# Kernel tuning notes

Measured on AMD Instinct MI355X. Metric: run time of the kernel, lower is better.

## Reference

```python
import jax, jax.numpy as jnp
import numpy as np

B, N, K = 4, 8192, 16
C_IN, C1, C2, C3 = 256, 128, 128, 64
WN = 8  # weight-net hidden channels

def _leaky(x):
    return jnp.where(x >= 0, x, 0.1 * x)

def _gather(x, idx):
    # x: [B, C, N], idx: [B, N, K] -> [B, C, N, K]
    return jax.vmap(lambda xb, ib: xb[:, ib])(x, idx)

def _point_conv(xyz, feat, knn, w_wn, b_wn, w_lin, b_lin):
    # xyz [B,3,N], feat [B,C,N] -> [B,out,N]
    f = jnp.concatenate([xyz, feat], axis=1)              # [B, C+3, N]
    fg = _gather(f, knn)                                  # [B, C+3, N, K]
    pos = _gather(xyz, knn) - xyz[:, :, :, None]          # [B, 3, N, K] relative coords
    w = _leaky(jnp.einsum('mc,bcnk->bmnk', w_wn, pos) + b_wn[None, :, None, None])  # [B,WN,N,K]
    agg = jnp.einsum('bcnk,bmnk->bncm', fg, w)            # [B, N, C+3, WN]
    agg = agg.reshape(agg.shape[0], agg.shape[1], -1)     # [B, N, (C+3)*WN]
    out = _leaky(jnp.einsum('bnf,of->bno', agg, w_lin) + b_lin)
    return out.transpose(0, 2, 1)                         # [B, out, N]

def _conv1x1(x, w, b):
    return jnp.einsum('oc,bcn->bon', w, x) + b[None, :, None]

def setup_inputs():
    key = jax.random.key(0)
    ks = jax.random.split(key, 16)
    def wn(k, shape, fan_in):
        return jax.random.normal(k, shape, jnp.float32) / np.sqrt(fan_in).astype(np.float32)
    return {
        'xyz': jax.random.normal(ks[0], (B, 3, N), jnp.float32),
        'feat': jax.random.normal(ks[1], (B, C_IN, N), jnp.float32),
        'knn_indices': jax.random.randint(ks[2], (B, N, K), 0, N, dtype=jnp.int32),
        'w_wn1': wn(ks[3], (WN, 3), 3), 'b_wn1': jnp.zeros((WN,), jnp.float32),
        'w_lin1': wn(ks[4], (C1, WN * (C_IN + 3)), WN * (C_IN + 3)), 'b_lin1': jnp.zeros((C1,), jnp.float32),
        'w_wn2': wn(ks[5], (WN, 3), 3), 'b_wn2': jnp.zeros((WN,), jnp.float32),
        'w_lin2': wn(ks[6], (C2, WN * (C1 + 3)), WN * (C1 + 3)), 'b_lin2': jnp.zeros((C2,), jnp.float32),
        'w_mlp1': wn(ks[7], (C2, C2), C2), 'b_mlp1': jnp.zeros((C2,), jnp.float32),
        'w_mlp2': wn(ks[8], (C3, C2), C2), 'b_mlp2': jnp.zeros((C3,), jnp.float32),
        'w_last': wn(ks[9], (3, C3), C3), 'b_last': jnp.zeros((3,), jnp.float32),
    }

def reference(xyz, feat, knn_indices, w_wn1, b_wn1, w_lin1, b_lin1,
              w_wn2, b_wn2, w_lin2, b_lin2, w_mlp1, b_mlp1,
              w_mlp2, b_mlp2, w_last, b_last):
    f = _point_conv(xyz, feat, knn_indices, w_wn1, b_wn1, w_lin1, b_lin1)
    f = _point_conv(xyz, f, knn_indices, w_wn2, b_wn2, w_lin2, b_lin2)
    f = _leaky(_conv1x1(f, w_mlp1, b_mlp1))
    f = _leaky(_conv1x1(f, w_mlp2, b_mlp2))   # flow_feat [B, 64, N]
    flow = _conv1x1(f, w_last, b_last)        # [B, 3, N]
    return (f, flow)
```

## Files before the change

### kernel.cpp

```cpp
#include <hip/hip_runtime.h>

#define NPTS 8192
#define PTS 32768

typedef unsigned short u16;
typedef __attribute__((ext_vector_type(8))) short bf16x8;
typedef __attribute__((ext_vector_type(4))) float f32x4;

__device__ __forceinline__ float lrelu(float x){ return x >= 0.f ? x : 0.1f*x; }
__device__ __forceinline__ unsigned f2bf(float x){
  unsigned u = __float_as_uint(x);
  return ((u + 0x7FFFu + ((u>>16)&1u)) >> 16);
}
__device__ __forceinline__ float bf2f(u16 h){ return __uint_as_float(((unsigned)h)<<16); }

__global__ __launch_bounds__(256) void xyz_fill_kernel(
    const float* __restrict__ xyz, u16* __restrict__ fT1, u16* __restrict__ fT2){
  long g = (long)blockIdx.x*256 + threadIdx.x;
  int b = (int)(g >> 13), n = (int)(g & 8191);
  unsigned v[3];
  #pragma unroll
  for (int j = 0; j < 3; ++j) v[j] = f2bf(xyz[((long)b*3 + j)*NPTS + n]);
  fT1[g*264 + 0] = (u16)v[0]; fT1[g*264 + 1] = (u16)v[1]; fT1[g*264 + 2] = (u16)v[2];
  #pragma unroll
  for (int j = 259; j < 264; ++j) fT1[g*264 + j] = 0;
  uint4 u;
  u.x = v[0] | (v[1] << 16);
  u.y = v[2];
  u.z = 0; u.w = 0;
  *(uint4*)(fT2 + g*136 + 128) = u;
}

__global__ __launch_bounds__(256) void transpose_feat_kernel(
    const float* __restrict__ feat, u16* __restrict__ fT1){
  __shared__ float tile[64][65];
  int bx = blockIdx.x, by = blockIdx.y, bz = blockIdx.z;
  int t = threadIdx.x;
  int x = t & 63, y4 = t >> 6;
  const float* src = feat + ((long)bz*256 + by*64)*NPTS + (long)bx*64;
  #pragma unroll
  for (int i = 0; i < 16; ++i){
    int c = y4 + i*4;
    tile[c][x] = src[(long)c*NPTS + x];
  }
  __syncthreads();
  u16* dst = fT1 + ((long)bz*NPTS + (long)bx*64)*264 + 3 + by*64;
  #pragma unroll
  for (int i = 0; i < 16; ++i){
    int p = y4 + i*4;
    dst[(long)p*264 + x] = (u16)f2bf(tile[x][p]);
  }
}

__global__ void prep_bt_kernel(const float* __restrict__ W, u16* __restrict__ Bt,
                               int KP, int KREAL){
  int o = blockIdx.y;
  int k = blockIdx.x*256 + threadIdx.x;
  if (k < KP)
    Bt[(long)o*KP + k] = (k < KREAL) ? (u16)f2bf(W[(long)o*KREAL + k]) : (u16)0;
}

__global__ void prep_bt2_kernel(const float* __restrict__ W, u16* __restrict__ Bt){
  int o = blockIdx.y;
  int k = blockIdx.x*256 + threadIdx.x;
  if (k >= 1088) return;
  int c = k >> 3, m = k & 7;
  u16 v = 0;
  if (c < 128)      v = (u16)f2bf(W[(long)o*1048 + (c+3)*8 + m]);
  else if (c < 131) v = (u16)f2bf(W[(long)o*1048 + (c-128)*8 + m]);
  Bt[(long)o*1088 + k] = v;
}

template<int S>
__global__ __launch_bounds__(256, 2) void fused_pc_kernel(
    const u16* __restrict__ fT, const float* __restrict__ xyz,
    const int* __restrict__ knn, const float* __restrict__ w_wn,
    const float* __restrict__ b_wn, const u16* __restrict__ Bt,
    const float* __restrict__ bias, u16* __restrict__ outp, int out_stride){
  constexpr int K   = S*8;
  constexpr int NCH = S/8;
  __shared__ __align__(16) u16   As[64][72];
  __shared__ __align__(16) u16   Bs[128][72];
  __shared__ __align__(16) float fst[64*140];
  __shared__ __align__(16) u16   wk2[64][16][8];

  int t = threadIdx.x;
  int cpx = (int)(gridDim.x >> 3);
  int swz = (blockIdx.x & 7)*cpx + (blockIdx.x >> 3);
  int m0 = swz*64;
  int b = m0 >> 13;
  long bbase = (long)b << 13;
  int n0 = m0 & 8191;

  int w = t >> 6, l = t & 63;
  int ln = l & 15, lh = l >> 4;
  int o0 = w*32;

  int p = l, kb = w;
  int4 iv = *(const int4*)(knn + ((long)(bbase + n0 + p))*16 + kb*4);
  int idxs[4] = {iv.x, iv.y, iv.z, iv.w};

  {
    float cx = xyz[((long)b*3+0)*NPTS + n0 + p];
    float cy = xyz[((long)b*3+1)*NPTS + n0 + p];
    float cz = xyz[((long)b*3+2)*NPTS + n0 + p];
    float wm[8][3], bm[8];
    #pragma unroll
    for (int m = 0; m < 8; ++m){
      wm[m][0] = w_wn[m*3+0]; wm[m][1] = w_wn[m*3+1]; wm[m][2] = w_wn[m*3+2];
      bm[m] = b_wn[m];
    }
    #pragma unroll
    for (int j = 0; j < 4; ++j){
      int k = kb*4 + j;
      int idx = idxs[j];
      float px = xyz[((long)b*3+0)*NPTS + idx] - cx;
      float py = xyz[((long)b*3+1)*NPTS + idx] - cy;
      float pz = xyz[((long)b*3+2)*NPTS + idx] - cz;
      unsigned wv[8];
      #pragma unroll
      for (int m = 0; m < 8; ++m){
        float v = wm[m][0]*px + wm[m][1]*py + wm[m][2]*pz + bm[m];
        wv[m] = f2bf(lrelu(v));
      }
      uint4 u;
      u.x = wv[0] | (wv[1] << 16);
      u.y = wv[2] | (wv[3] << 16);
      u.z = wv[4] | (wv[5] << 16);
      u.w = wv[6] | (wv[7] << 16);
      *(uint4*)&wk2[p][(k + p) & 15][0] = u;
    }
  }

  uint4 ga[4];
  #pragma unroll
  for (int j = 0; j < 4; ++j)
    ga[j] = *(const uint4*)(fT + (bbase + idxs[j])*(long)S + 0*8);

  int pA = w*16 + (l >> 2), cp = l & 3;

  f32x4 acc[4][2];
  #pragma unroll
  for (int i = 0; i < 4; ++i)
    #pragma unroll
    for (int j = 0; j < 2; ++j) acc[i][j] = (f32x4){0.f,0.f,0.f,0.f};

  for (int ch = 0; ch < NCH; ++ch){
    #pragma unroll
    for (int j = 0; j < 4; ++j){
      int k = kb*4 + j;
      uint4 v = ga[j];
      f32x4 lo, hi;
      lo[0] = bf2f((u16)(v.x & 0xffff)); lo[1] = bf2f((u16)(v.x >> 16));
      lo[2] = bf2f((u16)(v.y & 0xffff)); lo[3] = bf2f((u16)(v.y >> 16));
      hi[0] = bf2f((u16)(v.z & 0xffff)); hi[1] = bf2f((u16)(v.z >> 16));
      hi[2] = bf2f((u16)(v.w & 0xffff)); hi[3] = bf2f((u16)(v.w >> 16));
      *(f32x4*)&fst[p*140 + k*8 + 0] = lo;
      *(f32x4*)&fst[p*140 + k*8 + 4] = hi;
    }
    #pragma unroll
    for (int j = 0; j < 4; ++j){
      int idx2 = j*256 + t;
      int o = idx2 >> 3, seg = (idx2 & 7)*8;
      *(uint4*)&Bs[o][seg] = *(const uint4*)(Bt + (long)o*K + ch*64 + seg);
    }
    __syncthreads();

    if (ch + 1 < NCH){
      #pragma unroll
      for (int j = 0; j < 4; ++j)
        ga[j] = *(const uint4*)(fT + (bbase + idxs[j])*(long)S + (ch+1)*8);
    }

    {
      float a0[8], a1[8];
      #pragma unroll
      for (int m = 0; m < 8; ++m){ a0[m] = 0.f; a1[m] = 0.f; }
      #pragma unroll
      for (int k = 0; k < 16; ++k){
        bf16x8 wv = *(const bf16x8*)&wk2[pA][(k + pA) & 15][0];
        const float* fr = &fst[pA*140 + k*8 + cp*2];
        float f0 = fr[0], f1 = fr[1];
        #pragma unroll
        for (int m = 0; m < 8; ++m){
          float wf = bf2f((u16)wv[m]);
          a0[m] += f0*wf;
          a1[m] += f1*wf;
        }
      }
      uint4 u0, u1;
      u0.x = f2bf(a0[0]) | (f2bf(a0[1]) << 16);
      u0.y = f2bf(a0[2]) | (f2bf(a0[3]) << 16);
      u0.z = f2bf(a0[4]) | (f2bf(a0[5]) << 16);
      u0.w = f2bf(a0[6]) | (f2bf(a0[7]) << 16);
      u1.x = f2bf(a1[0]) | (f2bf(a1[1]) << 16);
      u1.y = f2bf(a1[2]) | (f2bf(a1[3]) << 16);
      u1.z = f2bf(a1[4]) | (f2bf(a1[5]) << 16);
      u1.w = f2bf(a1[6]) | (f2bf(a1[7]) << 16);
      *(uint4*)&As[pA][cp*16 + 0] = u0;
      *(uint4*)&As[pA][cp*16 + 8] = u1;
    }
    __syncthreads();

    #pragma unroll
    for (int kk = 0; kk < 2; ++kk){
      int koff = kk*32 + lh*8;
      bf16x8 af[4], bfr[2];
      #pragma unroll
      for (int fm = 0; fm < 4; ++fm)
        af[fm] = *(const bf16x8*)&As[fm*16 + ln][koff];
      #pragma unroll
      for (int fn = 0; fn < 2; ++fn)
        bfr[fn] = *(const bf16x8*)&Bs[o0 + fn*16 + ln][koff];
      #pragma unroll
      for (int fm = 0; fm < 4; ++fm)
        #pragma unroll
        for (int fn = 0; fn < 2; ++fn)
          acc[fm][fn] = __builtin_amdgcn_mfma_f32_16x16x32_bf16(af[fm], bfr[fn], acc[fm][fn], 0, 0, 0);
    }
    __syncthreads();
  }

  u16* Cs = (u16*)fst;
  float bia[2] = { bias[o0 + ln], bias[o0 + 16 + ln] };
  #pragma unroll
  for (int fm = 0; fm < 4; ++fm)
    #pragma unroll
    for (int fn = 0; fn < 2; ++fn)
      #pragma unroll
      for (int r = 0; r < 4; ++r){
        int row = fm*16 + lh*4 + r;
        int col = o0 + fn*16 + ln;
        Cs[row*128 + col] = (u16)f2bf(lrelu(acc[fm][fn][r] + bia[fn]));
      }
  __syncthreads();
  int r2 = t >> 2, s2 = t & 3;
  u16* dst = outp + (long)(m0 + r2)*out_stride + s2*32;
  #pragma unroll
  for (int q = 0; q < 4; ++q)
    *(uint4*)(dst + q*8) = *(uint4*)&Cs[r2*128 + s2*32 + q*8];
}

template<int BN, int OUTMODE>
__global__ __launch_bounds__(256) void mfma_lin_kernel(
    const u16* __restrict__ A, const u16* __restrict__ Bt,
    const float* __restrict__ bias, void* __restrict__ outp,
    int K, long chunk_base, int out_stride){
  __shared__ __align__(16) u16 As[64][72];
  __shared__ __align__(16) u16 Bs[BN][72];
  constexpr int FM = (BN == 128) ? 4 : 2;
  int t = threadIdx.x;
  int w = t >> 6, l = t & 63;
  int ln = l & 15, lh = l >> 4;
  int m0 = blockIdx.x * 64;
  int MOFF = (BN == 128) ? 0 : (w >> 1)*32;
  int o0   = (BN == 128) ? w*32 : (w & 1)*32;
  int srow = t >> 3;
  int scol = (t & 7) * 8;

  f32x4 acc[FM][2];
  #pragma unroll
  for (int i = 0; i < FM; ++i)
    #pragma unroll
    for (int j = 0; j < 2; ++j) acc[i][j] = (f32x4){0.f,0.f,0.f,0.f};

  int nkc = K >> 6;
  for (int kc = 0; kc < nkc; ++kc){
    uint4 a0 = *(const uint4*)(A + (long)(m0 + srow)*K      + kc*64 + scol);
    uint4 a1 = *(const uint4*)(A + (long)(m0 + srow + 32)*K + kc*64 + scol);
    uint4 bv[BN/32];
    #pragma unroll
    for (int r = 0; r < BN/32; ++r)
      bv[r] = *(const uint4*)(Bt + (long)(srow + r*32)*K + kc*64 + scol);
    __syncthreads();
    *(uint4*)&As[srow][scol]      = a0;
    *(uint4*)&As[srow + 32][scol] = a1;
    #pragma unroll
    for (int r = 0; r < BN/32; ++r)
      *(uint4*)&Bs[srow + r*32][scol] = bv[r];
    __syncthreads();
    #pragma unroll
    for (int kk = 0; kk < 2; ++kk){
      int koff = kk*32 + lh*8;
      bf16x8 af[FM], bfr[2];
      #pragma unroll
      for (int fm = 0; fm < FM; ++fm)
        af[fm] = *(const bf16x8*)&As[MOFF + fm*16 + ln][koff];
      #pragma unroll
      for (int fn = 0; fn < 2; ++fn)
        bfr[fn] = *(const bf16x8*)&Bs[o0 + fn*16 + ln][koff];
      #pragma unroll
      for (int fm = 0; fm < FM; ++fm)
        #pragma unroll
        for (int fn = 0; fn < 2; ++fn)
          acc[fm][fn] = __builtin_amdgcn_mfma_f32_16x16x32_bf16(af[fm], bfr[fn], acc[fm][fn], 0, 0, 0);
    }
    __syncthreads();
  }

  if (OUTMODE == 0){
    __shared__ u16 Cs[64*128];
    float bia[2];
    #pragma unroll
    for (int fn = 0; fn < 2; ++fn) bia[fn] = bias[o0 + fn*16 + ln];
    __syncthreads();
    #pragma unroll
    for (int fm = 0; fm < FM; ++fm)
      #pragma unroll
      for (int fn = 0; fn < 2; ++fn)
        #pragma unroll
        for (int r = 0; r < 4; ++r){
          int row = MOFF + fm*16 + lh*4 + r;
          int col = o0 + fn*16 + ln;
          Cs[row*128 + col] = (u16)f2bf(lrelu(acc[fm][fn][r] + bia[fn]));
        }
    __syncthreads();
    int r2 = t >> 2, s2 = t & 3;
    u16* dst = (u16*)outp + (chunk_base + m0 + r2)*(long)out_stride + s2*32;
    #pragma unroll
    for (int q = 0; q < 4; ++q)
      *(uint4*)(dst + q*8) = *(uint4*)&Cs[r2*128 + s2*32 + q*8];
  } else {
    float* outf = (float*)outp;
    #pragma unroll
    for (int fm = 0; fm < FM; ++fm)
      #pragma unroll
      for (int fn = 0; fn < 2; ++fn){
        long gp = chunk_base + m0 + MOFF + fm*16 + lh*4;
        int bb = (int)(gp >> 13), nn = (int)(gp & 8191);
        int col = o0 + fn*16 + ln;
        float bia = bias[col];
        float4 v;
        v.x = lrelu(acc[fm][fn][0] + bia);
        v.y = lrelu(acc[fm][fn][1] + bia);
        v.z = lrelu(acc[fm][fn][2] + bia);
        v.w = lrelu(acc[fm][fn][3] + bia);
        *(float4*)(outf + ((long)(bb*64 + col) << 13) + nn) = v;
      }
  }
}

__global__ __launch_bounds__(256) void flow_kernel(
    const float* __restrict__ f, const float* __restrict__ W,
    const float* __restrict__ bias, float* __restrict__ flow){
  long g = (long)blockIdx.x*256 + threadIdx.x;
  int b = (int)(g >> 13), n = (int)(g & 8191);
  float a0 = bias[0], a1 = bias[1], a2 = bias[2];
  const float* fb = f + (long)b*64*NPTS + n;
  #pragma unroll
  for (int c = 0; c < 64; ++c){
    float v = fb[(long)c*NPTS];
    a0 += v * W[c];
    a1 += v * W[64 + c];
    a2 += v * W[128 + c];
  }
  flow[((long)b*3 + 0)*NPTS + n] = a0;
  flow[((long)b*3 + 1)*NPTS + n] = a1;
  flow[((long)b*3 + 2)*NPTS + n] = a2;
}

extern "C" void kernel_launch(void* const* d_in, const int* in_sizes, int n_in,
                              void* d_out, int out_size, void* d_ws, size_t ws_size,
                              hipStream_t stream){
  const float* xyz    = (const float*)d_in[0];
  const float* feat   = (const float*)d_in[1];
  const int*   knn    = (const int*)  d_in[2];
  const float* w_wn1  = (const float*)d_in[3];
  const float* b_wn1  = (const float*)d_in[4];
  const float* w_lin1 = (const float*)d_in[5];
  const float* b_lin1 = (const float*)d_in[6];
  const float* w_wn2  = (const float*)d_in[7];
  const float* b_wn2  = (const float*)d_in[8];
  const float* w_lin2 = (const float*)d_in[9];
  const float* b_lin2 = (const float*)d_in[10];
  const float* w_mlp1 = (const float*)d_in[11];
  const float* b_mlp1 = (const float*)d_in[12];
  const float* w_mlp2 = (const float*)d_in[13];
  const float* b_mlp2 = (const float*)d_in[14];
  const float* w_last = (const float*)d_in[15];
  const float* b_last = (const float*)d_in[16];
  float* out = (float*)d_out;

  char* p = (char*)d_ws;
  auto carve = [&](size_t bytes)->char*{
    char* r = p; p += (bytes + 255) & ~(size_t)255; return r;
  };
  u16* fT1   = (u16*)carve((size_t)PTS*264*2);
  u16* fT2   = (u16*)carve((size_t)PTS*136*2);
  u16* Bt1   = (u16*)carve((size_t)128*2112*2);
  u16* Bt2   = (u16*)carve((size_t)128*1088*2);
  u16* Bm1   = (u16*)carve((size_t)128*128*2);
  u16* Bm2   = (u16*)carve((size_t)64*128*2);
  u16* feat2 = (u16*)carve((size_t)PTS*128*2);
  u16* h1    = (u16*)carve((size_t)PTS*128*2);

  xyz_fill_kernel<<<PTS/256, 256, 0, stream>>>(xyz, fT1, fT2);
  transpose_feat_kernel<<<dim3(128,4,4), 256, 0, stream>>>(feat, fT1);
  prep_bt_kernel<<<dim3(9,128), 256, 0, stream>>>(w_lin1, Bt1, 2112, 2072);
  prep_bt2_kernel<<<dim3(5,128), 256, 0, stream>>>(w_lin2, Bt2);
  prep_bt_kernel<<<dim3(1,128), 256, 0, stream>>>(w_mlp1, Bm1, 128, 128);
  prep_bt_kernel<<<dim3(1,64),  256, 0, stream>>>(w_mlp2, Bm2, 128, 128);

  fused_pc_kernel<264><<<PTS/64, 256, 0, stream>>>(fT1, xyz, knn, w_wn1, b_wn1, Bt1, b_lin1, fT2, 136);
  fused_pc_kernel<136><<<PTS/64, 256, 0, stream>>>(fT2, xyz, knn, w_wn2, b_wn2, Bt2, b_lin2, feat2, 128);

  mfma_lin_kernel<128,0><<<PTS/64, 256, 0, stream>>>(feat2, Bm1, b_mlp1, h1, 128, 0, 128);
  mfma_lin_kernel<64,1><<<PTS/64, 256, 0, stream>>>(h1, Bm2, b_mlp2, out, 128, 0, 0);
  flow_kernel<<<PTS/256, 256, 0, stream>>>(out, w_last, b_last, out + (long)4*64*NPTS);
}
```

Baseline: 330.8 us.

## Restructure fused point-conv aggregation with bf16 dot2, register B fragments, double-buffered A

Reworks the fused point-conv kernel so each thread gathers the neighbour features of its own point and keeps them as packed bf16 in shared memory, which removes the fp32 staging. The K-reduction now uses v_dot2_f32_bf16. B weight fragments are read straight from global memory into registers instead of being staged in shared memory. A is double-buffered so one barrier per chunk is dropped, s_setprio is raised around the MFMA block, launch bounds go to 3 blocks per CU, and 32-bit offsets are used. The aim is lower shared-memory footprint and traffic, fewer barriers and higher occupancy. In exchange there is more global load pressure for B and a possible change in bf16 rounding within the dot-product accumulation.

```diff
diff --git a/kernel.cpp b/kernel.cpp
--- a/kernel.cpp
+++ b/kernel.cpp
@@ -13,6 +13,14 @@
   return ((u + 0x7FFFu + ((u>>16)&1u)) >> 16);
 }
 __device__ __forceinline__ float bf2f(u16 h){ return __uint_as_float(((unsigned)h)<<16); }
+__device__ __forceinline__ unsigned packbf(float x, float y){
+  return f2bf(x) | (f2bf(y) << 16);
+}
+__device__ __forceinline__ float dot2bf(unsigned f, unsigned w, float c){
+  float d;
+  asm("v_dot2_f32_bf16 %0, %1, %2, %3" : "=v"(d) : "v"(f), "v"(w), "v"(c));
+  return d;
+}
 
 __global__ __launch_bounds__(256) void xyz_fill_kernel(
     const float* __restrict__ xyz, u16* __restrict__ fT1, u16* __restrict__ fT2){
@@ -72,33 +80,41 @@
 }
 
 template<int S>
-__global__ __launch_bounds__(256, 2) void fused_pc_kernel(
+__global__ __launch_bounds__(256, 3) void fused_pc3_kernel(
     const u16* __restrict__ fT, const float* __restrict__ xyz,
     const int* __restrict__ knn, const float* __restrict__ w_wn,
     const float* __restrict__ b_wn, const u16* __restrict__ Bt,
     const float* __restrict__ bias, u16* __restrict__ outp, int out_stride){
   constexpr int K   = S*8;
   constexpr int NCH = S/8;
-  __shared__ __align__(16) u16   As[64][72];
-  __shared__ __align__(16) u16   Bs[128][72];
-  __shared__ __align__(16) float fst[64*140];
-  __shared__ __align__(16) u16   wk2[64][16][8];
+  __shared__ __align__(16) unsigned fstw[64*68];
+  __shared__ __align__(16) unsigned wkw[64*68];
+  __shared__ __align__(16) u16 As[2][64][72];
 
   int t = threadIdx.x;
   int cpx = (int)(gridDim.x >> 3);
-  int swz = (blockIdx.x & 7)*cpx + (blockIdx.x >> 3);
+  int swz = ((int)blockIdx.x & 7)*cpx + ((int)blockIdx.x >> 3);
   int m0 = swz*64;
   int b = m0 >> 13;
-  long bbase = (long)b << 13;
+  int bbase = b << 13;
   int n0 = m0 & 8191;
-
   int w = t >> 6, l = t & 63;
   int ln = l & 15, lh = l >> 4;
-  int o0 = w*32;
-
-  int p = l, kb = w;
-  int4 iv = *(const int4*)(knn + ((long)(bbase + n0 + p))*16 + kb*4);
-  int idxs[4] = {iv.x, iv.y, iv.z, iv.w};
+  int oc0 = w*32;
+  int p  = w*16 + (l >> 2);
+  int kq = l & 3;
+
+  int4 iv = *(const int4*)(knn + ((long)(bbase + n0 + p))*16 + kq*4);
+  unsigned offs[4];
+  offs[0] = (unsigned)((bbase + iv.x)*S*2);
+  offs[1] = (unsigned)((bbase + iv.y)*S*2);
+  offs[2] = (unsigned)((bbase + iv.z)*S*2);
+  offs[3] = (unsigned)((bbase + iv.w)*S*2);
+
+  uint4 ga[4];
+  #pragma unroll
+  for (int j = 0; j < 4; ++j)
+    ga[j] = *(const uint4*)((const char*)fT + offs[j]);
 
   {
     float cx = xyz[((long)b*3+0)*NPTS + n0 + p];
@@ -110,119 +126,114 @@
       wm[m][0] = w_wn[m*3+0]; wm[m][1] = w_wn[m*3+1]; wm[m][2] = w_wn[m*3+2];
       bm[m] = b_wn[m];
     }
+    float wv[4][8];
+    int idq[4] = {iv.x, iv.y, iv.z, iv.w};
     #pragma unroll
     for (int j = 0; j < 4; ++j){
-      int k = kb*4 + j;
-      int idx = idxs[j];
-      float px = xyz[((long)b*3+0)*NPTS + idx] - cx;
-      float py = xyz[((long)b*3+1)*NPTS + idx] - cy;
-      float pz = xyz[((long)b*3+2)*NPTS + idx] - cz;
-      unsigned wv[8];
+      int id = idq[j];
+      float px = xyz[((long)b*3+0)*NPTS + id] - cx;
+      float py = xyz[((long)b*3+1)*NPTS + id] - cy;
+      float pz = xyz[((long)b*3+2)*NPTS + id] - cz;
+      #pragma unroll
+      for (int m = 0; m < 8; ++m)
+        wv[j][m] = lrelu(wm[m][0]*px + wm[m][1]*py + wm[m][2]*pz + bm[m]);
+    }
+    #pragma unroll
+    for (int m = 0; m < 8; ++m){
+      uint2 u;
+      u.x = packbf(wv[0][m], wv[1][m]);
+      u.y = packbf(wv[2][m], wv[3][m]);
+      *(uint2*)&wkw[p*68 + m*8 + kq*2] = u;
+    }
+  }
+
+  f32x4 acc[4][2];
+  #pragma unroll
+  for (int i = 0; i < 4; ++i)
+    #pragma unroll
+    for (int j = 0; j < 2; ++j) acc[i][j] = (f32x4){0.f,0.f,0.f,0.f};
+
+  for (int ch = 0; ch < NCH; ++ch){
+    #pragma unroll
+    for (int wd = 0; wd < 4; ++wd){
+      unsigned a0 = ((const unsigned*)&ga[0])[wd];
+      unsigned b0 = ((const unsigned*)&ga[1])[wd];
+      unsigned c0 = ((const unsigned*)&ga[2])[wd];
+      unsigned d0 = ((const unsigned*)&ga[3])[wd];
+      uint2 ue, uo;
+      ue.x = __builtin_amdgcn_perm(b0, a0, 0x05040100);
+      ue.y = __builtin_amdgcn_perm(d0, c0, 0x05040100);
+      uo.x = __builtin_amdgcn_perm(b0, a0, 0x07060302);
+      uo.y = __builtin_amdgcn_perm(d0, c0, 0x07060302);
+      *(uint2*)&fstw[p*68 + (2*wd)*8   + kq*2] = ue;
+      *(uint2*)&fstw[p*68 + (2*wd+1)*8 + kq*2] = uo;
+    }
+    if (ch + 1 < NCH){
+      #pragma unroll
+      for (int j = 0; j < 4; ++j)
+        ga[j] = *(const uint4*)((const char*)fT + offs[j] + (ch+1)*16);
+    }
+    uint4 bfr[2][2];
+    #pragma unroll
+    for (int kk = 0; kk < 2; ++kk)
+      #pragma unroll
+      for (int fn = 0; fn < 2; ++fn)
+        bfr[kk][fn] = *(const uint4*)(Bt + (long)(oc0 + fn*16 + ln)*K + ch*64 + kk*32 + lh*8);
+
+    int par = ch & 1;
+    {
+      int c0 = kq*2;
+      uint4 f0a = *(const uint4*)&fstw[p*68 + c0*8 + 0];
+      uint4 f0b = *(const uint4*)&fstw[p*68 + c0*8 + 4];
+      uint4 f1a = *(const uint4*)&fstw[p*68 + (c0+1)*8 + 0];
+      uint4 f1b = *(const uint4*)&fstw[p*68 + (c0+1)*8 + 4];
+      float a0[8], a1[8];
       #pragma unroll
       for (int m = 0; m < 8; ++m){
-        float v = wm[m][0]*px + wm[m][1]*py + wm[m][2]*pz + bm[m];
-        wv[m] = f2bf(lrelu(v));
-      }
-      uint4 u;
-      u.x = wv[0] | (wv[1] << 16);
-      u.y = wv[2] | (wv[3] << 16);
-      u.z = wv[4] | (wv[5] << 16);
-      u.w = wv[6] | (wv[7] << 16);
-      *(uint4*)&wk2[p][(k + p) & 15][0] = u;
-    }
-  }
-
-  uint4 ga[4];
-  #pragma unroll
-  for (int j = 0; j < 4; ++j)
-    ga[j] = *(const uint4*)(fT + (bbase + idxs[j])*(long)S + 0*8);
-
-  int pA = w*16 + (l >> 2), cp = l & 3;
-
-  f32x4 acc[4][2];
-  #pragma unroll
-  for (int i = 0; i < 4; ++i)
-    #pragma unroll
-    for (int j = 0; j < 2; ++j) acc[i][j] = (f32x4){0.f,0.f,0.f,0.f};
-
-  for (int ch = 0; ch < NCH; ++ch){
-    #pragma unroll
-    for (int j = 0; j < 4; ++j){
-      int k = kb*4 + j;
-      uint4 v = ga[j];
-      f32x4 lo, hi;
-      lo[0] = bf2f((u16)(v.x & 0xffff)); lo[1] = bf2f((u16)(v.x >> 16));
-      lo[2] = bf2f((u16)(v.y & 0xffff)); lo[3] = bf2f((u16)(v.y >> 16));
-      hi[0] = bf2f((u16)(v.z & 0xffff)); hi[1] = bf2f((u16)(v.z >> 16));
-      hi[2] = bf2f((u16)(v.w & 0xffff)); hi[3] = bf2f((u16)(v.w >> 16));
-      *(f32x4*)&fst[p*140 + k*8 + 0] = lo;
-      *(f32x4*)&fst[p*140 + k*8 + 4] = hi;
-    }
-    #pragma unroll
-    for (int j = 0; j < 4; ++j){
-      int idx2 = j*256 + t;
-      int o = idx2 >> 3, seg = (idx2 & 7)*8;
-      *(uint4*)&Bs[o][seg] = *(const uint4*)(Bt + (long)o*K + ch*64 + seg);
-    }
-    __syncthreads();
-
-    if (ch + 1 < NCH){
-      #pragma unroll
-      for (int j = 0; j < 4; ++j)
-        ga[j] = *(const uint4*)(fT + (bbase + idxs[j])*(long)S + (ch+1)*8);
-    }
-
-    {
-      float a0[8], a1[8];
-      #pragma unroll
-      for (int m = 0; m < 8; ++m){ a0[m] = 0.f; a1[m] = 0.f; }
-      #pragma unroll
-      for (int k = 0; k < 16; ++k){
-        bf16x8 wv = *(const bf16x8*)&wk2[pA][(k + pA) & 15][0];
-        const float* fr = &fst[pA*140 + k*8 + cp*2];
-        float f0 = fr[0], f1 = fr[1];
-        #pragma unroll
-        for (int m = 0; m < 8; ++m){
-          float wf = bf2f((u16)wv[m]);
-          a0[m] += f0*wf;
-          a1[m] += f1*wf;
-        }
+        uint4 wa = *(const uint4*)&wkw[p*68 + m*8 + 0];
+        uint4 wb = *(const uint4*)&wkw[p*68 + m*8 + 4];
+        float s0 = 0.f, s1 = 0.f;
+        s0 = dot2bf(f0a.x, wa.x, s0); s1 = dot2bf(f1a.x, wa.x, s1);
+        s0 = dot2bf(f0a.y, wa.y, s0); s1 = dot2bf(f1a.y, wa.y, s1);
+        s0 = dot2bf(f0a.z, wa.z, s0); s1 = dot2bf(f1a.z, wa.z, s1);
+        s0 = dot2bf(f0a.w, wa.w, s0); s1 = dot2bf(f1a.w, wa.w, s1);
+        s0 = dot2bf(f0b.x, wb.x, s0); s1 = dot2bf(f1b.x, wb.x, s1);
+        s0 = dot2bf(f0b.y, wb.y, s0); s1 = dot2bf(f1b.y, wb.y, s1);
+        s0 = dot2bf(f0b.z, wb.z, s0); s1 = dot2bf(f1b.z, wb.z, s1);
+        s0 = dot2bf(f0b.w, wb.w, s0); s1 = dot2bf(f1b.w, wb.w, s1);
+        a0[m] = s0; a1[m] = s1;
       }
       uint4 u0, u1;
-      u0.x = f2bf(a0[0]) | (f2bf(a0[1]) << 16);
-      u0.y = f2bf(a0[2]) | (f2bf(a0[3]) << 16);
-      u0.z = f2bf(a0[4]) | (f2bf(a0[5]) << 16);
-      u0.w = f2bf(a0[6]) | (f2bf(a0[7]) << 16);
-      u1.x = f2bf(a1[0]) | (f2bf(a1[1]) << 16);
-      u1.y = f2bf(a1[2]) | (f2bf(a1[3]) << 16);
-      u1.z = f2bf(a1[4]) | (f2bf(a1[5]) << 16);
-      u1.w = f2bf(a1[6]) | (f2bf(a1[7]) << 16);
-      *(uint4*)&As[pA][cp*16 + 0] = u0;
-      *(uint4*)&As[pA][cp*16 + 8] = u1;
-    }
-    __syncthreads();
-
+      u0.x = packbf(a0[0], a0[1]); u0.y = packbf(a0[2], a0[3]);
+      u0.z = packbf(a0[4], a0[5]); u0.w = packbf(a0[6], a0[7]);
+      u1.x = packbf(a1[0], a1[1]); u1.y = packbf(a1[2], a1[3]);
+      u1.z = packbf(a1[4], a1[5]); u1.w = packbf(a1[6], a1[7]);
+      *(uint4*)&As[par][p][kq*16 + 0] = u0;
+      *(uint4*)&As[par][p][kq*16 + 8] = u1;
+    }
+    __syncthreads();
+
+    __builtin_amdgcn_s_setprio(1);
     #pragma unroll
     for (int kk = 0; kk < 2; ++kk){
       int koff = kk*32 + lh*8;
-      bf16x8 af[4], bfr[2];
+      bf16x8 af[4];
       #pragma unroll
       for (int fm = 0; fm < 4; ++fm)
-        af[fm] = *(const bf16x8*)&As[fm*16 + ln][koff];
-      #pragma unroll
-      for (int fn = 0; fn < 2; ++fn)
-        bfr[fn] = *(const bf16x8*)&Bs[o0 + fn*16 + ln][koff];
-      #pragma unroll
-      for (int fm = 0; fm < 4; ++fm)
+        af[fm] = *(const bf16x8*)&As[par][fm*16 + ln][koff];
+      #pragma unroll
+      for (int fn = 0; fn < 2; ++fn){
+        bf16x8 bfrag = *(const bf16x8*)&bfr[kk][fn];
         #pragma unroll
-        for (int fn = 0; fn < 2; ++fn)
-          acc[fm][fn] = __builtin_amdgcn_mfma_f32_16x16x32_bf16(af[fm], bfr[fn], acc[fm][fn], 0, 0, 0);
-    }
-    __syncthreads();
-  }
-
-  u16* Cs = (u16*)fst;
-  float bia[2] = { bias[o0 + ln], bias[o0 + 16 + ln] };
+        for (int fm = 0; fm < 4; ++fm)
+          acc[fm][fn] = __builtin_amdgcn_mfma_f32_16x16x32_bf16(af[fm], bfrag, acc[fm][fn], 0, 0, 0);
+      }
+    }
+    __builtin_amdgcn_s_setprio(0);
+  }
+
+  u16* Cs = (u16*)fstw;
+  float bia[2] = { bias[oc0 + ln], bias[oc0 + 16 + ln] };
   #pragma unroll
   for (int fm = 0; fm < 4; ++fm)
     #pragma unroll
@@ -230,7 +241,7 @@
       #pragma unroll
       for (int r = 0; r < 4; ++r){
         int row = fm*16 + lh*4 + r;
-        int col = o0 + fn*16 + ln;
+        int col = oc0 + fn*16 + ln;
         Cs[row*128 + col] = (u16)f2bf(lrelu(acc[fm][fn][r] + bia[fn]));
       }
   __syncthreads();
@@ -401,8 +412,8 @@
   prep_bt_kernel<<<dim3(1,128), 256, 0, stream>>>(w_mlp1, Bm1, 128, 128);
   prep_bt_kernel<<<dim3(1,64),  256, 0, stream>>>(w_mlp2, Bm2, 128, 128);
 
-  fused_pc_kernel<264><<<PTS/64, 256, 0, stream>>>(fT1, xyz, knn, w_wn1, b_wn1, Bt1, b_lin1, fT2, 136);
-  fused_pc_kernel<136><<<PTS/64, 256, 0, stream>>>(fT2, xyz, knn, w_wn2, b_wn2, Bt2, b_lin2, feat2, 128);
+  fused_pc3_kernel<264><<<PTS/64, 256, 0, stream>>>(fT1, xyz, knn, w_wn1, b_wn1, Bt1, b_lin1, fT2, 136);
+  fused_pc3_kernel<136><<<PTS/64, 256, 0, stream>>>(fT2, xyz, knn, w_wn2, b_wn2, Bt2, b_lin2, feat2, 128);
 
   mfma_lin_kernel<128,0><<<PTS/64, 256, 0, stream>>>(feat2, Bm1, b_mlp1, h1, 128, 0, 128);
   mfma_lin_kernel<64,1><<<PTS/64, 256, 0, stream>>>(h1, Bm2, b_mlp2, out, 128, 0, 0);
```

After: 309.8 us. -6.3%, faster.
